# Kernel optimization log

Hardware: AMD Instinct MI355X
Metric: run time of the kernel (lower is better)

Reference implementation:

```python
import jax, jax.numpy as jnp
import numpy as np

NUM_HEADS = 16


def setup_inputs() -> dict:
    key = jax.random.key(0)
    ks = jax.random.split(key, 5)
    B, S, D = 2, 2048, 1024
    x = jax.random.normal(ks[0], (B, S, D), dtype=jnp.float32)
    # Linear weights stored torch-style as [out, in]; init scale ~ 1/sqrt(D)
    scale = 1.0 / np.sqrt(D)
    Wq = jax.random.uniform(ks[1], (D, D), jnp.float32, -scale, scale)
    bq = jax.random.uniform(ks[2], (D,), jnp.float32, -scale, scale)
    Wo = jax.random.uniform(ks[3], (D, D), jnp.float32, -scale, scale)
    bo = jax.random.uniform(ks[4], (D,), jnp.float32, -scale, scale)
    return {"x": x, "Wq": Wq, "bq": bq, "Wo": Wo, "bo": bo}


def reference(x, Wq, bq, Wo, bo):
    B, S, D = x.shape
    H = NUM_HEADS
    Hd = D // H
    # NOTE: faithful to the source bug — Q, K, V all use the *query* projection.
    q = x @ Wq.T + bq                       # [B,S,D]
    qh = q.reshape(B, S, H, Hd).transpose(0, 2, 1, 3)  # [B,H,S,Hd]
    scores = jnp.einsum('bhsd,bhtd->bhst', qh, qh) / jnp.sqrt(jnp.float32(Hd))
    weights = jax.nn.softmax(scores, axis=-1)          # [B,H,S,S]
    attn = jnp.einsum('bhst,bhtd->bhsd', weights, qh)  # [B,H,S,Hd]
    attn = attn.transpose(0, 2, 1, 3).reshape(B, S, D)
    return attn @ Wo.T + bo
```

## Files before the change

### kernel.cpp

```cpp
#include <hip/hip_runtime.h>
#include <hip/hip_bf16.h>

typedef __bf16 bf16x8 __attribute__((ext_vector_type(8)));
typedef float  f32x4  __attribute__((ext_vector_type(4)));
typedef float  f32x16 __attribute__((ext_vector_type(16)));

__device__ __forceinline__ void gload_lds16(const void* g, void* l) {
  __builtin_amdgcn_global_load_lds(
      (const __attribute__((address_space(1))) unsigned int*)g,
      (__attribute__((address_space(3))) unsigned int*)l, 16, 0, 0);
}

__device__ __forceinline__ void xcd_remap(int& x, int& y) {
  const int lin = blockIdx.x + (blockIdx.y << 4);
  const int xcd = lin & 7, slot = lin >> 3;
  y = ((slot >> 4) << 3) + xcd;
  x = slot & 15;
}

__global__ void k_cvt3(const float* __restrict__ x, const float* __restrict__ wq,
                       const float* __restrict__ wo, __bf16* __restrict__ xb,
                       __bf16* __restrict__ wqb, __bf16* __restrict__ wob) {
  const int i = blockIdx.x * 256 + threadIdx.x;
  const float* s; __bf16* d; int j;
  if (i < 1048576)      { s = x;  d = xb;  j = i; }
  else if (i < 1310720) { s = wq; d = wqb; j = i - 1048576; }
  else                  { s = wo; d = wob; j = i - 1310720; }
  float4 v = ((const float4*)s)[j];
  union { __bf16 h[4]; uint2 u; } o;
  o.h[0] = (__bf16)v.x; o.h[1] = (__bf16)v.y;
  o.h[2] = (__bf16)v.z; o.h[3] = (__bf16)v.w;
  ((uint2*)d)[j] = o.u;
}

template<bool OUT_BF16>
__global__ __launch_bounds__(256, 2)
void k_gemm_bt(const __bf16* __restrict__ A, const __bf16* __restrict__ B,
               const float* __restrict__ bias, void* __restrict__ C,
               int M, int N, int K) {
  __shared__ __align__(16) __bf16 At[4][128 * 32];
  __shared__ __align__(16) __bf16 Bt[4][64 * 32];
  const int tid  = threadIdx.x;
  const int lane = tid & 63;
  const int w    = tid >> 6;
  const int wr   = w >> 1, wc = w & 1;
  int bx, by; xcd_remap(bx, by);
  const int bm = by * 128, bn = bx * 64;

  f32x4 acc[4][2] = {};

  const __bf16* ga = A + (size_t)(bm + (tid >> 2)) * K + (tid & 3) * 8;
  const __bf16* gb = B + (size_t)(bn + (tid >> 2)) * K + (tid & 3) * 8;

#pragma unroll
  for (int p = 0; p < 2; ++p) {
    gload_lds16(ga + p * 32,                  &At[p][(w * 16) * 32]);
    gload_lds16(ga + p * 32 + (size_t)64 * K, &At[p][(64 + w * 16) * 32]);
    gload_lds16(gb + p * 32,                  &Bt[p][(w * 16) * 32]);
  }

  const int NIT = K / 32;
  for (int it = 0; it < NIT; ++it) {
    const int cur = it & 3;
    if (it + 2 < NIT) {
      const int nb = (it + 2) & 3;
      const int k2 = (it + 2) * 32;
      gload_lds16(ga + k2,                  &At[nb][(w * 16) * 32]);
      gload_lds16(ga + k2 + (size_t)64 * K, &At[nb][(64 + w * 16) * 32]);
      gload_lds16(gb + k2,                  &Bt[nb][(w * 16) * 32]);
      asm volatile("s_waitcnt vmcnt(6)" ::: "memory");
    } else if (it + 2 == NIT) {
      asm volatile("s_waitcnt vmcnt(3)" ::: "memory");
    } else {
      asm volatile("s_waitcnt vmcnt(0)" ::: "memory");
    }
    __builtin_amdgcn_s_barrier();
    __builtin_amdgcn_sched_barrier(0);

    bf16x8 a[4], b[2];
#pragma unroll
    for (int mt = 0; mt < 4; ++mt)
      a[mt] = *(const bf16x8*)&At[cur][(wr * 64 + mt * 16 + (lane & 15)) * 32 + (lane >> 4) * 8];
#pragma unroll
    for (int nt = 0; nt < 2; ++nt)
      b[nt] = *(const bf16x8*)&Bt[cur][(wc * 32 + nt * 16 + (lane & 15)) * 32 + (lane >> 4) * 8];
    __builtin_amdgcn_s_setprio(1);
#pragma unroll
    for (int mt = 0; mt < 4; ++mt)
#pragma unroll
      for (int nt = 0; nt < 2; ++nt)
        acc[mt][nt] = __builtin_amdgcn_mfma_f32_16x16x32_bf16(a[mt], b[nt], acc[mt][nt], 0, 0, 0);
    __builtin_amdgcn_s_setprio(0);
  }

#pragma unroll
  for (int nt = 0; nt < 2; ++nt) {
    const int col = bn + wc * 32 + nt * 16 + (lane & 15);
    const float bv = bias[col];
#pragma unroll
    for (int mt = 0; mt < 4; ++mt) {
#pragma unroll
      for (int r = 0; r < 4; ++r) {
        const int row = bm + wr * 64 + mt * 16 + (lane >> 4) * 4 + r;
        const float v = acc[mt][nt][r] + bv;
        if (OUT_BF16) ((__bf16*)C)[(size_t)row * N + col] = (__bf16)v;
        else          ((float*)C)[(size_t)row * N + col]  = v;
      }
    }
  }
}

#define SWZ2(row, col) ((row) * 64 + ((col) ^ (((((row) & 7) ^ ((row) >> 3)) & 7) << 3)))

#define ATTN_TILE(T, KB, VB)                                                  \
  {                                                                           \
    *(bf16x8*)&KB[SWZ2(2 * sm, c0)]     = v0;                                 \
    *(bf16x8*)&KB[SWZ2(2 * sm + 1, c0)] = v1;                                 \
    _Pragma("unroll")                                                         \
    for (int j = 0; j < 8; ++j) {                                             \
      union { __bf16 b[2]; unsigned u; } pk;                                  \
      pk.b[0] = v0[j]; pk.b[1] = v1[j];                                       \
      *(unsigned*)&VB[SWZ2(c0 + j, 2 * sm)] = pk.u;                           \
    }                                                                         \
    __syncthreads();                                                          \
    if ((T) < 31) {                                                           \
      v0 = *(const bf16x8*)&gsrc[(size_t)((T) + 1) * 64 * 1024];              \
      v1 = *(const bf16x8*)&gsrc[(size_t)((T) + 1) * 64 * 1024 + 1024];       \
    }                                                                         \
    f32x16 s[2] = {};                                                         \
    _Pragma("unroll")                                                         \
    for (int kvf = 0; kvf < 2; ++kvf) {                                       \
      __builtin_amdgcn_s_setprio(1);                                          \
      _Pragma("unroll")                                                       \
      for (int ks = 0; ks < 4; ++ks) {                                        \
        bf16x8 ka = *(const bf16x8*)&KB[SWZ2(kvf * 32 + l31, ks * 16 + h * 8)]; \
        s[kvf] = __builtin_amdgcn_mfma_f32_32x32x16_bf16(ka, qb[ks], s[kvf], 0, 0, 0); \
      }                                                                       \
      __builtin_amdgcn_s_setprio(0);                                          \
    }                                                                         \
    unsigned P[2][4][2];                                                      \
    _Pragma("unroll")                                                         \
    for (int kvf = 0; kvf < 2; ++kvf) {                                       \
      _Pragma("unroll")                                                       \
      for (int rq = 0; rq < 4; ++rq) {                                        \
        _Pragma("unroll")                                                     \
        for (int tt = 0; tt < 2; ++tt) {                                      \
          const float p0 = __builtin_amdgcn_exp2f(s[kvf][rq * 4 + tt * 2]);   \
          const float p1 = __builtin_amdgcn_exp2f(s[kvf][rq * 4 + tt * 2 + 1]); \
          union { __bf16 b[2]; unsigned u; } pk;                              \
          pk.b[0] = (__bf16)p0; pk.b[1] = (__bf16)p1;                         \
          P[kvf][rq][tt] = pk.u;                                              \
        }                                                                     \
      }                                                                       \
    }                                                                         \
    _Pragma("unroll")                                                         \
    for (int ko = 0; ko < 4; ++ko) {                                          \
      const int kvf = ko >> 1, rqa = (ko & 1) * 2, rqb = rqa + 1;             \
      asm volatile("v_permlane32_swap_b32 %0, %1"                             \
                   : "+v"(P[kvf][rqa][0]), "+v"(P[kvf][rqb][0]));             \
      asm volatile("v_permlane32_swap_b32 %0, %1"                             \
                   : "+v"(P[kvf][rqa][1]), "+v"(P[kvf][rqb][1]));             \
    }                                                                         \
    __builtin_amdgcn_s_setprio(1);                                            \
    _Pragma("unroll")                                                         \
    for (int ko = 0; ko < 4; ++ko) {                                          \
      const int kvf = ko >> 1, rqa = (ko & 1) * 2, rqb = rqa + 1;             \
      union { unsigned u[4]; bf16x8 v; } pu;                                  \
      pu.u[0] = P[kvf][rqa][0]; pu.u[1] = P[kvf][rqa][1];                     \
      pu.u[2] = P[kvf][rqb][0]; pu.u[3] = P[kvf][rqb][1];                     \
      Osum = __builtin_amdgcn_mfma_f32_32x32x16_bf16(pu.v, onesb, Osum, 0, 0, 0); \
      bf16x8 vb0 = *(const bf16x8*)&VB[SWZ2(l31,      ko * 16 + h * 8)];      \
      bf16x8 vb1 = *(const bf16x8*)&VB[SWZ2(32 + l31, ko * 16 + h * 8)];      \
      O[0] = __builtin_amdgcn_mfma_f32_32x32x16_bf16(pu.v, vb0, O[0], 0, 0, 0); \
      O[1] = __builtin_amdgcn_mfma_f32_32x32x16_bf16(pu.v, vb1, O[1], 0, 0, 0); \
    }                                                                         \
    __builtin_amdgcn_s_setprio(0);                                            \
  }

__global__ __launch_bounds__(256, 2)
void k_attn(const __bf16* __restrict__ q, __bf16* __restrict__ o) {
  __shared__ __align__(16) __bf16 Kt[2][64 * 64];
  __shared__ __align__(16) __bf16 Vt[2][64 * 64];
  const int tid = threadIdx.x, lane = tid & 63;
  const int w = tid >> 6;
  const int l31 = lane & 31, h = lane >> 5;
  int bqx, bh; xcd_remap(bqx, bh);
  const size_t base = ((size_t)(bh >> 4) * 2048) * 1024 + (bh & 15) * 64;
  const int q0 = bqx * 128 + w * 32;
  const float c2 = 0.18033688f;

  union { unsigned u[4]; bf16x8 v; } ones_u;
  ones_u.u[0] = 0x3F803F80u; ones_u.u[1] = 0x3F803F80u;
  ones_u.u[2] = 0x3F803F80u; ones_u.u[3] = 0x3F803F80u;
  const bf16x8 onesb = ones_u.v;

  bf16x8 qb[4];
#pragma unroll
  for (int ks = 0; ks < 4; ++ks) {
    union { bf16x8 v; __bf16 b[8]; } u;
    u.v = *(const bf16x8*)&q[base + (size_t)(q0 + l31) * 1024 + ks * 16 + h * 8];
#pragma unroll
    for (int j = 0; j < 8; ++j) u.b[j] = (__bf16)((float)u.b[j] * c2);
    qb[ks] = u.v;
  }

  f32x16 O[2] = {};
  f32x16 Osum = {};

  const int sm = tid >> 3, c0 = (tid & 7) * 8;
  const __bf16* gsrc = q + base + (size_t)(2 * sm) * 1024 + c0;

  __bf16* const K0 = &Kt[0][0];  __bf16* const V0 = &Vt[0][0];
  __bf16* const K1 = &Kt[1][0];  __bf16* const V1 = &Vt[1][0];

  bf16x8 v0 = *(const bf16x8*)&gsrc[0];
  bf16x8 v1 = *(const bf16x8*)&gsrc[1024];

  for (int t2 = 0; t2 < 16; ++t2) {
    ATTN_TILE(2 * t2,     K0, V0)
    ATTN_TILE(2 * t2 + 1, K1, V1)
  }

#pragma unroll
  for (int r = 0; r < 16; ++r) {
    const int qrow = (r & 3) + 8 * (r >> 2) + 4 * h;
    const float rs = 1.0f / Osum[r];
    o[base + (size_t)(q0 + qrow) * 1024 + l31]      = (__bf16)(O[0][r] * rs);
    o[base + (size_t)(q0 + qrow) * 1024 + 32 + l31] = (__bf16)(O[1][r] * rs);
  }
}

extern "C" void kernel_launch(void* const* d_in, const int* in_sizes, int n_in,
                              void* d_out, int out_size, void* d_ws, size_t ws_size,
                              hipStream_t stream) {
  const float* x  = (const float*)d_in[0];
  const float* Wq = (const float*)d_in[1];
  const float* bq = (const float*)d_in[2];
  const float* Wo = (const float*)d_in[3];
  const float* bo = (const float*)d_in[4];

  char* ws = (char*)d_ws;
  __bf16* xb  = (__bf16*)(ws);
  __bf16* ab  = (__bf16*)(ws);
  __bf16* wqb = (__bf16*)(ws + ((size_t)8  << 20));
  __bf16* wob = (__bf16*)(ws + ((size_t)10 << 20));
  __bf16* qb  = (__bf16*)(ws + ((size_t)12 << 20));

  const int M = 4096, N = 1024, K = 1024;

  k_cvt3<<<6144, 256, 0, stream>>>(x, Wq, Wo, xb, wqb, wob);

  k_gemm_bt<true ><<<dim3(16, 32), 256, 0, stream>>>(xb, wqb, bq, qb, M, N, K);
  k_attn          <<<dim3(16, 32), 256, 0, stream>>>(qb, ab);
  k_gemm_bt<false><<<dim3(16, 32), 256, 0, stream>>>(ab, wob, bo, d_out, M, N, K);
}
```

Baseline: 94.44 us.

## Process two query fragments per wave in attention to reuse K/V LDS reads

Each wave in the attention kernel now handles 64 query rows (two 32-row fragments) instead of 32, so each block covers 256 queries and the grid halves to 256 blocks. K and V fragments are loaded from LDS once into registers and reused across both query fragments, cutting LDS traffic and K/V tile loads per query. The cost is roughly doubled accumulator and register use, so launch bounds drop to one block per SM. With 256 blocks on a large GPU, occupancy and latency hiding may suffer.

```diff
diff --git a/kernel.cpp b/kernel.cpp
--- a/kernel.cpp
+++ b/kernel.cpp
@@ -127,66 +127,82 @@
       v0 = *(const bf16x8*)&gsrc[(size_t)((T) + 1) * 64 * 1024];              \
       v1 = *(const bf16x8*)&gsrc[(size_t)((T) + 1) * 64 * 1024 + 1024];       \
     }                                                                         \
-    f32x16 s[2] = {};                                                         \
-    _Pragma("unroll")                                                         \
-    for (int kvf = 0; kvf < 2; ++kvf) {                                       \
+    bf16x8 ka[2][4];                                                          \
+    _Pragma("unroll")                                                         \
+    for (int kvf = 0; kvf < 2; ++kvf)                                         \
+      _Pragma("unroll")                                                       \
+      for (int ks = 0; ks < 4; ++ks)                                          \
+        ka[kvf][ks] = *(const bf16x8*)&KB[SWZ2(kvf * 32 + l31, ks * 16 + h * 8)]; \
+    unsigned P[2][2][4][2];                                                   \
+    _Pragma("unroll")                                                         \
+    for (int qf = 0; qf < 2; ++qf) {                                          \
+      f32x16 s[2] = {};                                                       \
       __builtin_amdgcn_s_setprio(1);                                          \
       _Pragma("unroll")                                                       \
-      for (int ks = 0; ks < 4; ++ks) {                                        \
-        bf16x8 ka = *(const bf16x8*)&KB[SWZ2(kvf * 32 + l31, ks * 16 + h * 8)]; \
-        s[kvf] = __builtin_amdgcn_mfma_f32_32x32x16_bf16(ka, qb[ks], s[kvf], 0, 0, 0); \
-      }                                                                       \
+      for (int kvf = 0; kvf < 2; ++kvf)                                       \
+        _Pragma("unroll")                                                     \
+        for (int ks = 0; ks < 4; ++ks)                                        \
+          s[kvf] = __builtin_amdgcn_mfma_f32_32x32x16_bf16(ka[kvf][ks], qb[qf][ks], s[kvf], 0, 0, 0); \
       __builtin_amdgcn_s_setprio(0);                                          \
-    }                                                                         \
-    unsigned P[2][4][2];                                                      \
-    _Pragma("unroll")                                                         \
-    for (int kvf = 0; kvf < 2; ++kvf) {                                       \
-      _Pragma("unroll")                                                       \
-      for (int rq = 0; rq < 4; ++rq) {                                        \
+      _Pragma("unroll")                                                       \
+      for (int kvf = 0; kvf < 2; ++kvf) {                                     \
         _Pragma("unroll")                                                     \
-        for (int tt = 0; tt < 2; ++tt) {                                      \
-          const float p0 = __builtin_amdgcn_exp2f(s[kvf][rq * 4 + tt * 2]);   \
-          const float p1 = __builtin_amdgcn_exp2f(s[kvf][rq * 4 + tt * 2 + 1]); \
-          union { __bf16 b[2]; unsigned u; } pk;                              \
-          pk.b[0] = (__bf16)p0; pk.b[1] = (__bf16)p1;                         \
-          P[kvf][rq][tt] = pk.u;                                              \
+        for (int rq = 0; rq < 4; ++rq) {                                      \
+          _Pragma("unroll")                                                   \
+          for (int tt = 0; tt < 2; ++tt) {                                    \
+            const float p0 = __builtin_amdgcn_exp2f(s[kvf][rq * 4 + tt * 2]); \
+            const float p1 = __builtin_amdgcn_exp2f(s[kvf][rq * 4 + tt * 2 + 1]); \
+            union { __bf16 b[2]; unsigned u; } pk;                            \
+            pk.b[0] = (__bf16)p0; pk.b[1] = (__bf16)p1;                       \
+            P[qf][kvf][rq][tt] = pk.u;                                        \
+          }                                                                   \
         }                                                                     \
       }                                                                       \
-    }                                                                         \
-    _Pragma("unroll")                                                         \
-    for (int ko = 0; ko < 4; ++ko) {                                          \
-      const int kvf = ko >> 1, rqa = (ko & 1) * 2, rqb = rqa + 1;             \
-      asm volatile("v_permlane32_swap_b32 %0, %1"                             \
-                   : "+v"(P[kvf][rqa][0]), "+v"(P[kvf][rqb][0]));             \
-      asm volatile("v_permlane32_swap_b32 %0, %1"                             \
-                   : "+v"(P[kvf][rqa][1]), "+v"(P[kvf][rqb][1]));             \
-    }                                                                         \
+      _Pragma("unroll")                                                       \
+      for (int ko = 0; ko < 4; ++ko) {                                        \
+        const int kvf = ko >> 1, rqa = (ko & 1) * 2, rqb = rqa + 1;           \
+        asm volatile("v_permlane32_swap_b32 %0, %1"                           \
+                     : "+v"(P[qf][kvf][rqa][0]), "+v"(P[qf][kvf][rqb][0]));   \
+        asm volatile("v_permlane32_swap_b32 %0, %1"                           \
+                     : "+v"(P[qf][kvf][rqa][1]), "+v"(P[qf][kvf][rqb][1]));   \
+      }                                                                       \
+    }                                                                         \
+    bf16x8 vb[2][4];                                                          \
+    _Pragma("unroll")                                                         \
+    for (int dh = 0; dh < 2; ++dh)                                            \
+      _Pragma("unroll")                                                       \
+      for (int ko = 0; ko < 4; ++ko)                                          \
+        vb[dh][ko] = *(const bf16x8*)&VB[SWZ2(dh * 32 + l31, ko * 16 + h * 8)]; \
     __builtin_amdgcn_s_setprio(1);                                            \
     _Pragma("unroll")                                                         \
-    for (int ko = 0; ko < 4; ++ko) {                                          \
-      const int kvf = ko >> 1, rqa = (ko & 1) * 2, rqb = rqa + 1;             \
-      union { unsigned u[4]; bf16x8 v; } pu;                                  \
-      pu.u[0] = P[kvf][rqa][0]; pu.u[1] = P[kvf][rqa][1];                     \
-      pu.u[2] = P[kvf][rqb][0]; pu.u[3] = P[kvf][rqb][1];                     \
-      Osum = __builtin_amdgcn_mfma_f32_32x32x16_bf16(pu.v, onesb, Osum, 0, 0, 0); \
-      bf16x8 vb0 = *(const bf16x8*)&VB[SWZ2(l31,      ko * 16 + h * 8)];      \
-      bf16x8 vb1 = *(const bf16x8*)&VB[SWZ2(32 + l31, ko * 16 + h * 8)];      \
-      O[0] = __builtin_amdgcn_mfma_f32_32x32x16_bf16(pu.v, vb0, O[0], 0, 0, 0); \
-      O[1] = __builtin_amdgcn_mfma_f32_32x32x16_bf16(pu.v, vb1, O[1], 0, 0, 0); \
+    for (int qf = 0; qf < 2; ++qf) {                                          \
+      _Pragma("unroll")                                                       \
+      for (int ko = 0; ko < 4; ++ko) {                                        \
+        const int kvf = ko >> 1, rqa = (ko & 1) * 2, rqb = rqa + 1;           \
+        union { unsigned u[4]; bf16x8 v; } pu;                                \
+        pu.u[0] = P[qf][kvf][rqa][0]; pu.u[1] = P[qf][kvf][rqa][1];           \
+        pu.u[2] = P[qf][kvf][rqb][0]; pu.u[3] = P[qf][kvf][rqb][1];           \
+        Osum[qf] = __builtin_amdgcn_mfma_f32_32x32x16_bf16(pu.v, onesb, Osum[qf], 0, 0, 0); \
+        O[qf][0] = __builtin_amdgcn_mfma_f32_32x32x16_bf16(pu.v, vb[0][ko], O[qf][0], 0, 0, 0); \
+        O[qf][1] = __builtin_amdgcn_mfma_f32_32x32x16_bf16(pu.v, vb[1][ko], O[qf][1], 0, 0, 0); \
+      }                                                                       \
     }                                                                         \
     __builtin_amdgcn_s_setprio(0);                                            \
   }
 
-__global__ __launch_bounds__(256, 2)
+__global__ __launch_bounds__(256, 1)
 void k_attn(const __bf16* __restrict__ q, __bf16* __restrict__ o) {
   __shared__ __align__(16) __bf16 Kt[2][64 * 64];
   __shared__ __align__(16) __bf16 Vt[2][64 * 64];
   const int tid = threadIdx.x, lane = tid & 63;
   const int w = tid >> 6;
   const int l31 = lane & 31, h = lane >> 5;
-  int bqx, bh; xcd_remap(bqx, bh);
+  const int lin = blockIdx.x + (blockIdx.y << 3);
+  const int xcd = lin & 7, slot = lin >> 3;
+  const int bh = xcd + 8 * (slot >> 3);
+  const int bqx = slot & 7;
   const size_t base = ((size_t)(bh >> 4) * 2048) * 1024 + (bh & 15) * 64;
-  const int q0 = bqx * 128 + w * 32;
+  const int q0 = bqx * 256 + w * 64;
   const float c2 = 0.18033688f;
 
   union { unsigned u[4]; bf16x8 v; } ones_u;
@@ -194,18 +210,20 @@
   ones_u.u[2] = 0x3F803F80u; ones_u.u[3] = 0x3F803F80u;
   const bf16x8 onesb = ones_u.v;
 
-  bf16x8 qb[4];
-#pragma unroll
-  for (int ks = 0; ks < 4; ++ks) {
-    union { bf16x8 v; __bf16 b[8]; } u;
-    u.v = *(const bf16x8*)&q[base + (size_t)(q0 + l31) * 1024 + ks * 16 + h * 8];
-#pragma unroll
-    for (int j = 0; j < 8; ++j) u.b[j] = (__bf16)((float)u.b[j] * c2);
-    qb[ks] = u.v;
-  }
-
-  f32x16 O[2] = {};
-  f32x16 Osum = {};
+  bf16x8 qb[2][4];
+#pragma unroll
+  for (int qf = 0; qf < 2; ++qf)
+#pragma unroll
+    for (int ks = 0; ks < 4; ++ks) {
+      union { bf16x8 v; __bf16 b[8]; } u;
+      u.v = *(const bf16x8*)&q[base + (size_t)(q0 + qf * 32 + l31) * 1024 + ks * 16 + h * 8];
+#pragma unroll
+      for (int j = 0; j < 8; ++j) u.b[j] = (__bf16)((float)u.b[j] * c2);
+      qb[qf][ks] = u.v;
+    }
+
+  f32x16 O[2][2] = {};
+  f32x16 Osum[2] = {};
 
   const int sm = tid >> 3, c0 = (tid & 7) * 8;
   const __bf16* gsrc = q + base + (size_t)(2 * sm) * 1024 + c0;
@@ -222,11 +240,14 @@
   }
 
 #pragma unroll
-  for (int r = 0; r < 16; ++r) {
-    const int qrow = (r & 3) + 8 * (r >> 2) + 4 * h;
-    const float rs = 1.0f / Osum[r];
-    o[base + (size_t)(q0 + qrow) * 1024 + l31]      = (__bf16)(O[0][r] * rs);
-    o[base + (size_t)(q0 + qrow) * 1024 + 32 + l31] = (__bf16)(O[1][r] * rs);
+  for (int qf = 0; qf < 2; ++qf) {
+#pragma unroll
+    for (int r = 0; r < 16; ++r) {
+      const int qrow = (r & 3) + 8 * (r >> 2) + 4 * h;
+      const float rs = 1.0f / Osum[qf][r];
+      o[base + (size_t)(q0 + qf * 32 + qrow) * 1024 + l31]      = (__bf16)(O[qf][0][r] * rs);
+      o[base + (size_t)(q0 + qf * 32 + qrow) * 1024 + 32 + l31] = (__bf16)(O[qf][1][r] * rs);
+    }
   }
 }
 
@@ -251,6 +272,6 @@
   k_cvt3<<<6144, 256, 0, stream>>>(x, Wq, Wo, xb, wqb, wob);
 
   k_gemm_bt<true ><<<dim3(16, 32), 256, 0, stream>>>(xb, wqb, bq, qb, M, N, K);
-  k_attn          <<<dim3(16, 32), 256, 0, stream>>>(qb, ab);
+  k_attn          <<<dim3(8, 32), 256, 0, stream>>>(qb, ab);
   k_gemm_bt<false><<<dim3(16, 32), 256, 0, stream>>>(ab, wob, bo, d_out, M, N, K);
 }
```

Result: slower. 103.5 us (+9.6%).

## Process two KV tiles per barrier phase with quad-buffered LDS

Applied to the files above, without the earlier changes.

The attention loop now stages two 64-row K/V tiles into LDS per phase and computes both before the next barrier, so it needs half as many __syncthreads calls. Global prefetch now loads two tiles ahead into four register vectors, and LDS grows to four K and four V buffers. This trades more LDS (64KB per block) and more registers for fewer synchronisations, and it may reduce occupancy below the two blocks per CU requested in launch bounds.

```diff
diff --git a/kernel.cpp b/kernel.cpp
--- a/kernel.cpp
+++ b/kernel.cpp
@@ -112,21 +112,18 @@
 
 #define SWZ2(row, col) ((row) * 64 + ((col) ^ (((((row) & 7) ^ ((row) >> 3)) & 7) << 3)))
 
-#define ATTN_TILE(T, KB, VB)                                                  \
-  {                                                                           \
-    *(bf16x8*)&KB[SWZ2(2 * sm, c0)]     = v0;                                 \
-    *(bf16x8*)&KB[SWZ2(2 * sm + 1, c0)] = v1;                                 \
+#define WRITE_TILE(KB, VB, va, vb2)                                           \
+    *(bf16x8*)&KB[SWZ2(2 * sm, c0)]     = va;                                 \
+    *(bf16x8*)&KB[SWZ2(2 * sm + 1, c0)] = vb2;                                \
     _Pragma("unroll")                                                         \
     for (int j = 0; j < 8; ++j) {                                             \
       union { __bf16 b[2]; unsigned u; } pk;                                  \
-      pk.b[0] = v0[j]; pk.b[1] = v1[j];                                       \
+      pk.b[0] = va[j]; pk.b[1] = vb2[j];                                      \
       *(unsigned*)&VB[SWZ2(c0 + j, 2 * sm)] = pk.u;                           \
-    }                                                                         \
-    __syncthreads();                                                          \
-    if ((T) < 31) {                                                           \
-      v0 = *(const bf16x8*)&gsrc[(size_t)((T) + 1) * 64 * 1024];              \
-      v1 = *(const bf16x8*)&gsrc[(size_t)((T) + 1) * 64 * 1024 + 1024];       \
-    }                                                                         \
+    }
+
+#define COMPUTE_TILE(KB, VB)                                                  \
+  {                                                                           \
     f32x16 s[2] = {};                                                         \
     _Pragma("unroll")                                                         \
     for (int kvf = 0; kvf < 2; ++kvf) {                                       \
@@ -177,10 +174,25 @@
     __builtin_amdgcn_s_setprio(0);                                            \
   }
 
+#define PHASE(T, KA, VA, KB, VB)                                              \
+  {                                                                           \
+    WRITE_TILE(KA, VA, v0, v1)                                                \
+    WRITE_TILE(KB, VB, v2, v3)                                                \
+    __syncthreads();                                                          \
+    if ((T) < 30) {                                                           \
+      v0 = *(const bf16x8*)&gsrc[(size_t)((T) + 2) * 64 * 1024];              \
+      v1 = *(const bf16x8*)&gsrc[(size_t)((T) + 2) * 64 * 1024 + 1024];       \
+      v2 = *(const bf16x8*)&gsrc[(size_t)((T) + 3) * 64 * 1024];              \
+      v3 = *(const bf16x8*)&gsrc[(size_t)((T) + 3) * 64 * 1024 + 1024];       \
+    }                                                                         \
+    COMPUTE_TILE(KA, VA)                                                      \
+    COMPUTE_TILE(KB, VB)                                                      \
+  }
+
 __global__ __launch_bounds__(256, 2)
 void k_attn(const __bf16* __restrict__ q, __bf16* __restrict__ o) {
-  __shared__ __align__(16) __bf16 Kt[2][64 * 64];
-  __shared__ __align__(16) __bf16 Vt[2][64 * 64];
+  __shared__ __align__(16) __bf16 Kt[4][64 * 64];
+  __shared__ __align__(16) __bf16 Vt[4][64 * 64];
   const int tid = threadIdx.x, lane = tid & 63;
   const int w = tid >> 6;
   const int l31 = lane & 31, h = lane >> 5;
@@ -212,13 +224,17 @@
 
   __bf16* const K0 = &Kt[0][0];  __bf16* const V0 = &Vt[0][0];
   __bf16* const K1 = &Kt[1][0];  __bf16* const V1 = &Vt[1][0];
+  __bf16* const K2 = &Kt[2][0];  __bf16* const V2 = &Vt[2][0];
+  __bf16* const K3 = &Kt[3][0];  __bf16* const V3 = &Vt[3][0];
 
   bf16x8 v0 = *(const bf16x8*)&gsrc[0];
   bf16x8 v1 = *(const bf16x8*)&gsrc[1024];
-
-  for (int t2 = 0; t2 < 16; ++t2) {
-    ATTN_TILE(2 * t2,     K0, V0)
-    ATTN_TILE(2 * t2 + 1, K1, V1)
+  bf16x8 v2 = *(const bf16x8*)&gsrc[64 * 1024];
+  bf16x8 v3 = *(const bf16x8*)&gsrc[64 * 1024 + 1024];
+
+  for (int p2 = 0; p2 < 8; ++p2) {
+    PHASE(4 * p2,     K0, V0, K1, V1)
+    PHASE(4 * p2 + 2, K2, V2, K3, V3)
   }
 
 #pragma unroll
```

Result: no change. 94.06 us (median of 2 runs) (-0.4%).
